# Kernel optimization log

Hardware: AMD Instinct MI355X
Metric: run time of the kernel (lower is better)

## Reference

```python
import jax, jax.numpy as jnp
import numpy as np

N_NODES = 50000
N_RAND_EDGES = 800000
LEAKY_SLOPE = 0.2


def gat_layer(x, edge_index, W, a_src, a_dst, b, num_heads):
    """Multi-head GAT layer. W: [Din, Dout]; heads split Dout; concat output."""
    N = x.shape[0]
    Dout = W.shape[1]
    Dh = Dout // num_heads
    z = (x @ W).reshape(N, num_heads, Dh)                      # [N,H,Dh]
    src = edge_index[0]
    dst = edge_index[1]
    alpha_src = jnp.einsum('nhd,hd->nh', z, a_src)             # [N,H]
    alpha_dst = jnp.einsum('nhd,hd->nh', z, a_dst)             # [N,H]
    e = jax.nn.leaky_relu(alpha_src[src] + alpha_dst[dst], LEAKY_SLOPE)  # [E,H]
    # segment softmax over incoming edges of each dst node
    m = jax.ops.segment_max(e, dst, num_segments=N)            # [N,H]
    e = jnp.exp(e - m[dst])
    denom = jax.ops.segment_sum(e, dst, num_segments=N)        # [N,H]
    alpha = e / (denom[dst] + 1e-16)                           # [E,H]
    msg = z[src] * alpha[:, :, None]                           # [E,H,Dh]
    out = jax.ops.segment_sum(msg, dst, num_segments=N)        # [N,H,Dh]
    return out.reshape(N, Dout) + b


def setup_inputs() -> dict:
    key = jax.random.key(0)
    ks = jax.random.split(key, 12)
    input_dim, hidden_dim, num_classes, num_heads = 128, 64, 16, 8
    x = jax.random.normal(ks[0], (N_NODES, input_dim), dtype=jnp.float32)
    rand_edges = jax.random.randint(ks[1], (2, N_RAND_EDGES), 0, N_NODES, dtype=jnp.int32)
    self_loops = jnp.tile(jnp.arange(N_NODES, dtype=jnp.int32), (2, 1))
    edge_indices = jnp.concatenate([rand_edges, self_loops], axis=1)   # [2, 850000]

    def glorot(k, shape):
        fan = sum(shape[-2:]) if len(shape) > 1 else shape[0]
        return jax.random.normal(k, shape, dtype=jnp.float32) * (2.0 / fan) ** 0.5

    W1 = glorot(ks[2], (input_dim, hidden_dim))
    a_src1 = glorot(ks[3], (num_heads, hidden_dim // num_heads))
    a_dst1 = glorot(ks[4], (num_heads, hidden_dim // num_heads))
    b1 = jnp.zeros((hidden_dim,), dtype=jnp.float32)
    W2 = glorot(ks[5], (hidden_dim, num_classes))
    a_src2 = glorot(ks[6], (1, num_classes))
    a_dst2 = glorot(ks[7], (1, num_classes))
    b2 = jnp.zeros((num_classes,), dtype=jnp.float32)
    return {"x": x, "edge_indices": edge_indices,
            "W1": W1, "a_src1": a_src1, "a_dst1": a_dst1, "b1": b1,
            "W2": W2, "a_src2": a_src2, "a_dst2": a_dst2, "b2": b2}


def reference(x, edge_indices, W1, a_src1, a_dst1, b1, W2, a_src2, a_dst2, b2):
    # Dropout is identity in eval mode.
    h = gat_layer(x, edge_indices, W1, a_src1, a_dst1, b1, num_heads=8)
    h = jax.nn.elu(h)
    return gat_layer(h, edge_indices, W2, a_src2, a_dst2, b2, num_heads=1)
```

## Files before the change

kernel.cpp:

```cpp
#include <hip/hip_runtime.h>
#include <hip/hip_fp16.h>


#define LRELU(v) ((v) > 0.f ? (v) : 0.2f * (v))

#define NB   196
#define BCAP 5120

__global__ void __launch_bounds__(256, 4)
kA(const float* __restrict__ x, const float* __restrict__ W1,
   const float* __restrict__ a_dst1,
   const int* __restrict__ src, const int* __restrict__ dst,
   int* __restrict__ bcnt, int* __restrict__ pairs,
   __half* __restrict__ z1h, float* __restrict__ ad1, int N, int E) {
    __shared__ float xs[64][133];
    __shared__ float avs[64];
    int b = blockIdx.x;
    int tid = threadIdx.x;
    bool is_part = ((b % 5) == 4);

    if (is_part) {
        int* hist  = (int*)&xs[0][0];
        int* base_ = hist + 256;
        int* cur   = hist + 512;
        int rank = b / 5;
        if (tid < NB) hist[tid] = 0;
        __syncthreads();
        int chunk = (E + NB - 1) / NB;
        int e0 = rank * chunk;
        int e1 = min(e0 + chunk, E);
        for (int e = e0 + tid; e < e1; e += 256)
            atomicAdd(&hist[dst[e] >> 8], 1);
        __syncthreads();
        if (tid < NB) {
            base_[tid] = atomicAdd(&bcnt[tid], hist[tid]);
            cur[tid] = 0;
        }
        __syncthreads();
        for (int e = e0 + tid; e < e1; e += 256) {
            int d = dst[e], s = src[e];
            int bk = d >> 8;
            int r = atomicAdd(&cur[bk], 1);
            int idx = base_[bk] + r;
            if (idx < BCAP) pairs[bk * BCAP + idx] = (s << 8) | (d & 255);
        }
        return;
    }

    int tile = (b / 5) * 4 + (b % 5);
    if (tile >= 782) return;
    int n0 = tile * 64;
    for (int idx = tid; idx < 2048; idx += 256) {
        int r = idx >> 5, q = idx & 31;
        int n = n0 + r; if (n >= N) n = N - 1;
        float4 v = ((const float4*)(x + (size_t)n * 128))[q];
        *(float4*)&xs[r][q * 4] = v;
    }
    if (tid < 64) avs[tid] = a_dst1[tid];
    __syncthreads();

    int rg = tid >> 4, cg2 = tid & 15;
    int xr = rg * 4;
    const float4* wb = (const float4*)W1 + cg2;
    float acc[4][4] = {};
    float4 xv[4], wl[4];
#pragma unroll
    for (int i = 0; i < 4; ++i) xv[i] = *(const float4*)&xs[xr + i][0];
#pragma unroll
    for (int kk = 0; kk < 4; ++kk) wl[kk] = wb[kk * 16];
#pragma unroll 2
    for (int k4 = 0; k4 < 32; ++k4) {
        float4 xn[4], wn[4];
        int kn = (k4 + 1) & 31;
#pragma unroll
        for (int i = 0; i < 4; ++i) xn[i] = *(const float4*)&xs[xr + i][kn * 4];
#pragma unroll
        for (int kk = 0; kk < 4; ++kk) wn[kk] = wb[(kn * 4 + kk) * 16];
#pragma unroll
        for (int i = 0; i < 4; ++i) {
            acc[i][0] += xv[i].x * wl[0].x; acc[i][1] += xv[i].x * wl[0].y;
            acc[i][2] += xv[i].x * wl[0].z; acc[i][3] += xv[i].x * wl[0].w;
            acc[i][0] += xv[i].y * wl[1].x; acc[i][1] += xv[i].y * wl[1].y;
            acc[i][2] += xv[i].y * wl[1].z; acc[i][3] += xv[i].y * wl[1].w;
            acc[i][0] += xv[i].z * wl[2].x; acc[i][1] += xv[i].z * wl[2].y;
            acc[i][2] += xv[i].z * wl[2].z; acc[i][3] += xv[i].z * wl[2].w;
            acc[i][0] += xv[i].w * wl[3].x; acc[i][1] += xv[i].w * wl[3].y;
            acc[i][2] += xv[i].w * wl[3].z; acc[i][3] += xv[i].w * wl[3].w;
        }
#pragma unroll
        for (int i = 0; i < 4; ++i) { xv[i] = xn[i]; wl[i] = wn[i]; }
    }
    int h = cg2 >> 1, db = (cg2 & 1) * 4;
    float pad_[4];
#pragma unroll
    for (int i = 0; i < 4; ++i) {
        float dd = 0.f;
#pragma unroll
        for (int j = 0; j < 4; ++j) dd += acc[i][j] * avs[h * 8 + db + j];
        pad_[i] = dd;
    }
#pragma unroll
    for (int i = 0; i < 4; ++i)
        pad_[i] += __shfl_xor(pad_[i], 1, 64);
#pragma unroll
    for (int i = 0; i < 4; ++i) {
        int n = n0 + rg * 4 + i;
        if (n < N) {
            union { __half2 h2[2]; uint2 u; } pk;
            pk.h2[0] = __floats2half2_rn(acc[i][0], acc[i][1]);
            pk.h2[1] = __floats2half2_rn(acc[i][2], acc[i][3]);
            *(uint2*)&z1h[(size_t)n * 64 + cg2 * 4] = pk.u;
            if ((cg2 & 1) == 0) ad1[(size_t)n * 8 + h] = pad_[i];
        }
    }
}

__global__ void kB(const int* __restrict__ bcnt, const int* __restrict__ pairs,
                   int* __restrict__ deg, int* __restrict__ csr, int N) {
    __shared__ int cur[256];
    int b = blockIdx.x;
    int tid = threadIdx.x;
    cur[tid] = 0;
    __syncthreads();
    int nb = min(bcnt[b], BCAP);
    const int* p = pairs + b * BCAP;
    for (int i = tid; i < nb; i += 256) {
        int v = p[i];
        int off = v & 255, s = v >> 8;
        int r = atomicAdd(&cur[off], 1);
        if (r < 64) csr[(((b << 8) + off) << 6) + r] = s;
    }
    __syncthreads();
    int d = (b << 8) + tid;
    if (d < N) deg[d] = cur[tid];
}

__global__ void kg1(const int* __restrict__ deg, const int* __restrict__ csr,
                    const float* __restrict__ a_src1, const float* __restrict__ ad1,
                    const __half* __restrict__ z1h, const float* __restrict__ b1,
                    const float* __restrict__ W2, const float* __restrict__ a_src2,
                    const float* __restrict__ a_dst2,
                    float* __restrict__ z2r, int N) {
    __shared__ int s_idx[16][65];
    __shared__ int sdeg[16];
    __shared__ float hs[4][4][68];
    __shared__ float ws2[64][18];
    int tid = threadIdx.x;
    int lane = tid & 63, wid = tid >> 6;
    int blk0 = blockIdx.x * 16;
    for (int i = tid; i < 1024; i += 256) ws2[i >> 4][i & 15] = W2[i];
    for (int idx = tid; idx < 1024; idx += 256) {
        int dl = idx >> 6, sl = idx & 63;
        int dr = blk0 + dl; if (dr >= N) dr = N - 1;
        s_idx[dl][sl] = csr[(dr << 6) + sl];
    }
    if (tid < 16) {
        int dr = blk0 + tid; if (dr >= N) dr = N - 1;
        sdeg[tid] = min(deg[dr], 64);
    }
    __syncthreads();

    int dloc = lane >> 4, g = (lane >> 3) & 1, q = lane & 7;
    int dl16 = wid * 4 + dloc;
    int d = blk0 + dl16;
    int dc = d < N ? d : N - 1;
    int cnt = d < N ? sdeg[dl16] : 0;
    float adv = ad1[(size_t)dc * 8 + q];
    float4 asA = *(const float4*)(a_src1 + q * 8);
    float4 asB = *(const float4*)(a_src1 + q * 8 + 4);
    float a0 = 0.f, a1 = 0.f, a2 = 0.f, a3 = 0.f;
    float a4 = 0.f, a5 = 0.f, a6 = 0.f, a7 = 0.f, dsum = 0.f;
#pragma unroll 2
    for (int j = g; j < cnt; j += 2) {
        int s = s_idx[dl16][j];
        float4 raw = *(const float4*)(z1h + (size_t)s * 64 + q * 8);
        const __half2* hp = (const __half2*)&raw;
        float2 f0 = __half22float2(hp[0]), f1 = __half22float2(hp[1]);
        float2 f2 = __half22float2(hp[2]), f3 = __half22float2(hp[3]);
        float av = f0.x * asA.x + f0.y * asA.y + f1.x * asA.z + f1.y * asA.w
                 + f2.x * asB.x + f2.y * asB.y + f3.x * asB.z + f3.y * asB.w;
        float ev = av + adv;
        float w = __expf(LRELU(ev));
        a0 += w * f0.x; a1 += w * f0.y; a2 += w * f1.x; a3 += w * f1.y;
        a4 += w * f2.x; a5 += w * f2.y; a6 += w * f3.x; a7 += w * f3.y;
        dsum += w;
    }
    a0 += __shfl_xor(a0, 8, 64); a1 += __shfl_xor(a1, 8, 64);
    a2 += __shfl_xor(a2, 8, 64); a3 += __shfl_xor(a3, 8, 64);
    a4 += __shfl_xor(a4, 8, 64); a5 += __shfl_xor(a5, 8, 64);
    a6 += __shfl_xor(a6, 8, 64); a7 += __shfl_xor(a7, 8, 64);
    dsum += __shfl_xor(dsum, 8, 64);
    float inv = cnt ? 1.f / dsum : 0.f;
    float4 bv0 = *(const float4*)(b1 + q * 8);
    float4 bv1 = *(const float4*)(b1 + q * 8 + 4);
    float hv[8] = {a0 * inv + bv0.x, a1 * inv + bv0.y,
                   a2 * inv + bv0.z, a3 * inv + bv0.w,
                   a4 * inv + bv1.x, a5 * inv + bv1.y,
                   a6 * inv + bv1.z, a7 * inv + bv1.w};
#pragma unroll
    for (int i = 0; i < 8; ++i) hv[i] = hv[i] > 0.f ? hv[i] : expm1f(hv[i]);
    if (g == 0) {
        *(float4*)&hs[wid][dloc][q * 8]     = make_float4(hv[0], hv[1], hv[2], hv[3]);
        *(float4*)&hs[wid][dloc][q * 8 + 4] = make_float4(hv[4], hv[5], hv[6], hv[7]);
    }
    float zc0 = 0.f, zc1 = 0.f;
#pragma unroll
    for (int k4 = 0; k4 < 16; ++k4) {
        float4 hh = *(const float4*)&hs[wid][dloc][k4 * 4];
        float2 w0 = *(const float2*)&ws2[k4 * 4 + 0][q * 2];
        float2 w1 = *(const float2*)&ws2[k4 * 4 + 1][q * 2];
        float2 w2 = *(const float2*)&ws2[k4 * 4 + 2][q * 2];
        float2 w3 = *(const float2*)&ws2[k4 * 4 + 3][q * 2];
        zc0 += hh.x * w0.x; zc1 += hh.x * w0.y;
        zc0 += hh.y * w1.x; zc1 += hh.y * w1.y;
        zc0 += hh.z * w2.x; zc1 += hh.z * w2.y;
        zc0 += hh.w * w3.x; zc1 += hh.w * w3.y;
    }
    if (g == 0 && d < N)
        *(float2*)&z2r[(size_t)d * 32 + q * 2] = make_float2(zc0, zc1);
    float ps = zc0 * a_src2[q * 2] + zc1 * a_src2[q * 2 + 1];
    float pd = zc0 * a_dst2[q * 2] + zc1 * a_dst2[q * 2 + 1];
#pragma unroll
    for (int m = 1; m < 8; m <<= 1) {
        ps += __shfl_xor(ps, m, 64);
        pd += __shfl_xor(pd, m, 64);
    }
    if (q == 0 && g == 0 && d < N) {
        z2r[(size_t)d * 32 + 16] = ps;
        z2r[(size_t)d * 32 + 17] = pd;
    }
}

__global__ void kg2(const int* __restrict__ deg, const int* __restrict__ csr,
                    const float* __restrict__ z2r, const float* __restrict__ b2,
                    float* __restrict__ out, int N) {
    __shared__ int s_idx[16][65];
    __shared__ int sdeg[16];
    int tid = threadIdx.x;
    int lane = tid & 63, wid = tid >> 6;
    int blk0 = blockIdx.x * 16;
    for (int idx = tid; idx < 1024; idx += 256) {
        int dl = idx >> 6, sl = idx & 63;
        int dr = blk0 + dl; if (dr >= N) dr = N - 1;
        s_idx[dl][sl] = csr[(dr << 6) + sl];
    }
    if (tid < 16) {
        int dr = blk0 + tid; if (dr >= N) dr = N - 1;
        sdeg[tid] = min(deg[dr], 64);
    }
    __syncthreads();

    int dloc = lane >> 4, g = (lane >> 2) & 3, c = lane & 3;
    int dl16 = wid * 4 + dloc;
    int d = blk0 + dl16;
    int dc = d < N ? d : N - 1;
    int cnt = d < N ? sdeg[dl16] : 0;
    float adv = z2r[(size_t)dc * 32 + 17];
    float ax = 0.f, ay = 0.f, az = 0.f, aw = 0.f, dsum = 0.f;
#pragma unroll 2
    for (int j = g; j < cnt; j += 4) {
        int s = s_idx[dl16][j];
        float as2v = z2r[(size_t)s * 32 + 16];
        float ev = as2v + adv;
        float w = __expf(LRELU(ev));
        float4 zv = *(const float4*)(z2r + (size_t)s * 32 + c * 4);
        ax += w * zv.x; ay += w * zv.y; az += w * zv.z; aw += w * zv.w;
        dsum += w;
    }
#pragma unroll
    for (int m = 4; m <= 8; m <<= 1) {
        ax += __shfl_xor(ax, m, 64); ay += __shfl_xor(ay, m, 64);
        az += __shfl_xor(az, m, 64); aw += __shfl_xor(aw, m, 64);
        dsum += __shfl_xor(dsum, m, 64);
    }
    if (g == 0 && d < N) {
        float inv = 1.f / dsum;
        float4 o = make_float4(ax * inv + b2[c * 4], ay * inv + b2[c * 4 + 1],
                               az * inv + b2[c * 4 + 2], aw * inv + b2[c * 4 + 3]);
        *(float4*)&out[(size_t)d * 16 + c * 4] = o;
    }
}

extern "C" void kernel_launch(void* const* d_in, const int* in_sizes, int n_in,
                              void* d_out, int out_size, void* d_ws, size_t ws_size,
                              hipStream_t stream) {
    const float* x      = (const float*)d_in[0];
    const int*   ei     = (const int*)d_in[1];
    const float* W1     = (const float*)d_in[2];
    const float* a_src1 = (const float*)d_in[3];
    const float* a_dst1 = (const float*)d_in[4];
    const float* b1     = (const float*)d_in[5];
    const float* W2     = (const float*)d_in[6];
    const float* a_src2 = (const float*)d_in[7];
    const float* a_dst2 = (const float*)d_in[8];
    const float* b2     = (const float*)d_in[9];
    float* out = (float*)d_out;

    const int N = in_sizes[0] / 128;
    const int E = in_sizes[1] / 2;
    const int* src = ei;
    const int* dst = ei + E;

    float* ws = (float*)d_ws;
    size_t off = 0;
    __half* z1h = (__half*)(ws + off); off += (size_t)N * 32;
    float* ad1 = ws + off; off += (size_t)N * 8;
    float* z2r = ws + off; off += (size_t)N * 32;
    int* csr = (int*)(ws + off); off += (size_t)N * 64;
    int* deg = (int*)(ws + off); off += (size_t)N;
    int* pairs = (int*)(ws + off); off += (size_t)NB * BCAP;
    int* bcnt = (int*)(ws + off); off += NB;

    hipMemsetAsync(bcnt, 0, (size_t)NB * sizeof(int), stream);

    kA<<<980, 256, 0, stream>>>(x, W1, a_dst1, src, dst, bcnt, pairs,
                                z1h, ad1, N, E);
    kB<<<NB, 256, 0, stream>>>(bcnt, pairs, deg, csr, N);
    kg1<<<(N + 15) / 16, 256, 0, stream>>>(deg, csr, a_src1, ad1, z1h, b1, W2,
                                           a_src2, a_dst2, z2r, N);
    kg2<<<(N + 15) / 16, 256, 0, stream>>>(deg, csr, z2r, b2, out, N);
}
```

Measured before the change: 163.1 us.

## Compute first-layer projection with fp16 MFMA instead of FP32 FMA loop

Replaces the scalar FP32 register-tiled x@W1 GEMM in kA with MFMA 16x16x32 fp16 instructions. x and a transposed W1 are converted to half precision and staged in shared memory, and the attention-dst dot product is recomputed from the MFMA accumulator layout with lane shuffles. This cuts the ALU cost of the projection but rounds the inputs to fp16 and adds conversion and transpose work when loading tiles.

After: 158.3 us (median of 2 runs). 1.03x faster.

```diff
diff --git a/kernel.cpp b/kernel.cpp
--- a/kernel.cpp
+++ b/kernel.cpp
@@ -6,6 +6,9 @@
 
 #define NB   196
 #define BCAP 5120
+
+typedef _Float16 f16x8 __attribute__((ext_vector_type(8)));
+typedef float f32x4 __attribute__((ext_vector_type(4)));
 
 __global__ void __launch_bounds__(256, 4)
 kA(const float* __restrict__ x, const float* __restrict__ W1,
@@ -13,14 +16,15 @@
    const int* __restrict__ src, const int* __restrict__ dst,
    int* __restrict__ bcnt, int* __restrict__ pairs,
    __half* __restrict__ z1h, float* __restrict__ ad1, int N, int E) {
-    __shared__ float xs[64][133];
+    __shared__ __half xsh[64][136];
+    __shared__ __half wtT[64][136];
     __shared__ float avs[64];
     int b = blockIdx.x;
     int tid = threadIdx.x;
     bool is_part = ((b % 5) == 4);
 
     if (is_part) {
-        int* hist  = (int*)&xs[0][0];
+        int* hist  = (int*)&xsh[0][0];
         int* base_ = hist + 256;
         int* cur   = hist + 512;
         int rank = b / 5;
@@ -54,63 +58,62 @@
         int r = idx >> 5, q = idx & 31;
         int n = n0 + r; if (n >= N) n = N - 1;
         float4 v = ((const float4*)(x + (size_t)n * 128))[q];
-        *(float4*)&xs[r][q * 4] = v;
+        union { __half2 h2[2]; uint2 u; } pk;
+        pk.h2[0] = __floats2half2_rn(v.x, v.y);
+        pk.h2[1] = __floats2half2_rn(v.z, v.w);
+        *(uint2*)&xsh[r][q * 4] = pk.u;
+    }
+    for (int idx = tid; idx < 1024; idx += 256) {
+        int kp = idx >> 4, cq = idx & 15;
+        float4 va = ((const float4*)(W1 + (size_t)(kp * 2) * 64))[cq];
+        float4 vb = ((const float4*)(W1 + (size_t)(kp * 2 + 1) * 64))[cq];
+        int c = cq * 4;
+        *(__half2*)&wtT[c + 0][kp * 2] = __floats2half2_rn(va.x, vb.x);
+        *(__half2*)&wtT[c + 1][kp * 2] = __floats2half2_rn(va.y, vb.y);
+        *(__half2*)&wtT[c + 2][kp * 2] = __floats2half2_rn(va.z, vb.z);
+        *(__half2*)&wtT[c + 3][kp * 2] = __floats2half2_rn(va.w, vb.w);
     }
     if (tid < 64) avs[tid] = a_dst1[tid];
     __syncthreads();
 
-    int rg = tid >> 4, cg2 = tid & 15;
-    int xr = rg * 4;
-    const float4* wb = (const float4*)W1 + cg2;
-    float acc[4][4] = {};
-    float4 xv[4], wl[4];
-#pragma unroll
-    for (int i = 0; i < 4; ++i) xv[i] = *(const float4*)&xs[xr + i][0];
-#pragma unroll
-    for (int kk = 0; kk < 4; ++kk) wl[kk] = wb[kk * 16];
-#pragma unroll 2
-    for (int k4 = 0; k4 < 32; ++k4) {
-        float4 xn[4], wn[4];
-        int kn = (k4 + 1) & 31;
-#pragma unroll
-        for (int i = 0; i < 4; ++i) xn[i] = *(const float4*)&xs[xr + i][kn * 4];
-#pragma unroll
-        for (int kk = 0; kk < 4; ++kk) wn[kk] = wb[(kn * 4 + kk) * 16];
-#pragma unroll
-        for (int i = 0; i < 4; ++i) {
-            acc[i][0] += xv[i].x * wl[0].x; acc[i][1] += xv[i].x * wl[0].y;
-            acc[i][2] += xv[i].x * wl[0].z; acc[i][3] += xv[i].x * wl[0].w;
-            acc[i][0] += xv[i].y * wl[1].x; acc[i][1] += xv[i].y * wl[1].y;
-            acc[i][2] += xv[i].y * wl[1].z; acc[i][3] += xv[i].y * wl[1].w;
-            acc[i][0] += xv[i].z * wl[2].x; acc[i][1] += xv[i].z * wl[2].y;
-            acc[i][2] += xv[i].z * wl[2].z; acc[i][3] += xv[i].z * wl[2].w;
-            acc[i][0] += xv[i].w * wl[3].x; acc[i][1] += xv[i].w * wl[3].y;
-            acc[i][2] += xv[i].w * wl[3].z; acc[i][3] += xv[i].w * wl[3].w;
+    int lane = tid & 63, wv = tid >> 6;
+    int rsub = lane & 15, kg = lane >> 4;
+    f32x4 acc0 = {0.f, 0.f, 0.f, 0.f}, acc1 = {0.f, 0.f, 0.f, 0.f};
+    f32x4 acc2 = {0.f, 0.f, 0.f, 0.f}, acc3 = {0.f, 0.f, 0.f, 0.f};
+#pragma unroll
+    for (int k0 = 0; k0 < 128; k0 += 32) {
+        f16x8 av = *(const f16x8*)&xsh[wv * 16 + rsub][k0 + kg * 8];
+        f16x8 b0 = *(const f16x8*)&wtT[rsub][k0 + kg * 8];
+        f16x8 b1 = *(const f16x8*)&wtT[16 + rsub][k0 + kg * 8];
+        f16x8 b2 = *(const f16x8*)&wtT[32 + rsub][k0 + kg * 8];
+        f16x8 b3 = *(const f16x8*)&wtT[48 + rsub][k0 + kg * 8];
+        acc0 = __builtin_amdgcn_mfma_f32_16x16x32_f16(av, b0, acc0, 0, 0, 0);
+        acc1 = __builtin_amdgcn_mfma_f32_16x16x32_f16(av, b1, acc1, 0, 0, 0);
+        acc2 = __builtin_amdgcn_mfma_f32_16x16x32_f16(av, b2, acc2, 0, 0, 0);
+        acc3 = __builtin_amdgcn_mfma_f32_16x16x32_f16(av, b3, acc3, 0, 0, 0);
+    }
+#pragma unroll
+    for (int reg = 0; reg < 4; ++reg) {
+        int n = n0 + wv * 16 + kg * 4 + reg;
+        if (n < N) {
+            __half* zp = z1h + (size_t)n * 64 + rsub;
+            zp[0]  = __float2half_rn(acc0[reg]);
+            zp[16] = __float2half_rn(acc1[reg]);
+            zp[32] = __float2half_rn(acc2[reg]);
+            zp[48] = __float2half_rn(acc3[reg]);
         }
-#pragma unroll
-        for (int i = 0; i < 4; ++i) { xv[i] = xn[i]; wl[i] = wn[i]; }
-    }
-    int h = cg2 >> 1, db = (cg2 & 1) * 4;
-    float pad_[4];
-#pragma unroll
-    for (int i = 0; i < 4; ++i) {
-        float dd = 0.f;
-#pragma unroll
-        for (int j = 0; j < 4; ++j) dd += acc[i][j] * avs[h * 8 + db + j];
-        pad_[i] = dd;
-    }
-#pragma unroll
-    for (int i = 0; i < 4; ++i)
-        pad_[i] += __shfl_xor(pad_[i], 1, 64);
-#pragma unroll
-    for (int i = 0; i < 4; ++i) {
-        int n = n0 + rg * 4 + i;
-        if (n < N) {
-            union { __half2 h2[2]; uint2 u; } pk;
-            pk.h2[0] = __floats2half2_rn(acc[i][0], acc[i][1]);
-            pk.h2[1] = __floats2half2_rn(acc[i][2], acc[i][3]);
-            *(uint2*)&z1h[(size_t)n * 64 + cg2 * 4] = pk.u;
-            if ((cg2 & 1) == 0) ad1[(size_t)n * 8 + h] = pad_[i];
+        float v0 = acc0[reg] * avs[rsub];
+        float v1 = acc1[reg] * avs[16 + rsub];
+        float v2 = acc2[reg] * avs[32 + rsub];
+        float v3 = acc3[reg] * avs[48 + rsub];
+        v0 += __shfl_xor(v0, 1, 64); v0 += __shfl_xor(v0, 2, 64); v0 += __shfl_xor(v0, 4, 64);
+        v1 += __shfl_xor(v1, 1, 64); v1 += __shfl_xor(v1, 2, 64); v1 += __shfl_xor(v1, 4, 64);
+        v2 += __shfl_xor(v2, 1, 64); v2 += __shfl_xor(v2, 2, 64); v2 += __shfl_xor(v2, 4, 64);
+        v3 += __shfl_xor(v3, 1, 64); v3 += __shfl_xor(v3, 2, 64); v3 += __shfl_xor(v3, 4, 64);
+        if ((rsub & 7) == 0 && n < N) {
+            int hi = rsub >> 3;
+            float* ap = ad1 + (size_t)n * 8 + hi;
+            ap[0] = v0; ap[2] = v1; ap[4] = v2; ap[6] = v3;
         }
     }
 }
```
